# Kernel tuning notes

Measured on AMD Instinct MI355X. Metric: run time of the kernel, lower is better.

## Reference

```python
import jax, jax.numpy as jnp
import numpy as np

EPS = 1e-4
MAX_LAPLACE_VAR = 1000.0
MAX_DENSITY = 10000.0
BINS = 256

_LAP_KERNEL = jnp.array([[0., 1., 0.], [1., -4., 1.], [0., 1., 0.]], dtype=jnp.float32)[None, None]  # OIHW [1,1,3,3]


def setup_inputs() -> dict:
    key = jax.random.key(0)
    k1, k2 = jax.random.split(key)
    rgb_img = jax.random.uniform(k1, (32, 3, 512, 512), dtype=jnp.float32)
    depth_img = jax.random.normal(k2, (32, 1, 512, 512), dtype=jnp.float32)
    return {"rgb_img": rgb_img, "depth_img": depth_img}


def _rgb_confidence(rgb_img):
    B, C, H, W = rgb_img.shape
    gray = 0.299 * rgb_img[:, 0] + 0.587 * rgb_img[:, 1] + 0.114 * rgb_img[:, 2]  # [B,H,W]
    gray = gray[:, None]  # [B,1,H,W]
    lap = jax.lax.conv_general_dilated(
        gray, _LAP_KERNEL, window_strides=(1, 1), padding=[(1, 1), (1, 1)],
        dimension_numbers=("NCHW", "OIHW", "NCHW"))
    # torch.var default is unbiased (ddof=1)
    laplace_var = jnp.var(lap, axis=(1, 2, 3), ddof=1)

    # integer-valued pixels 0..255 land exactly in histc bins 0..255 (bins=256, min=0, max=255)
    vals = jnp.clip(gray * 255.0, 0.0, 255.0).astype(jnp.int32)  # [B,1,H,W]
    vals = vals.reshape(B, -1)  # [B, H*W]
    bidx = jnp.broadcast_to(jnp.arange(B)[:, None], vals.shape)
    hist = jnp.zeros((B, BINS), jnp.float32).at[bidx, vals].add(1.0)
    p = hist / jnp.sum(hist, axis=1, keepdims=True)
    entropy = -jnp.sum(p * jnp.log2(p + EPS), axis=1)

    clarity_score = laplace_var / (MAX_LAPLACE_VAR + EPS)
    uniformity_score = 1.0 / (entropy + EPS)
    return (0.5 * (clarity_score + uniformity_score))[:, None]  # [B,1]


def _depth_confidence(depth_img):
    C = depth_img.shape[1]
    depth_map = depth_img[:, 2] if C == 3 else depth_img[:, 0]  # [B,H,W]
    mask = (depth_map > 0).astype(jnp.float32)
    density = jnp.mean(mask, axis=(1, 2))

    # vectorized masked std (unbiased, ddof=1), matching torch.std over valid pixels
    n = jnp.sum(mask, axis=(1, 2))  # [B]
    mean = jnp.sum(depth_map * mask, axis=(1, 2)) / jnp.maximum(n, 1.0)
    sq = jnp.sum(mask * (depth_map - mean[:, None, None]) ** 2, axis=(1, 2))
    var = sq / jnp.maximum(n - 1.0, 1.0)
    std = jnp.sqrt(jnp.maximum(var, 0.0))
    noise_level = jnp.where(n > 0, std, 1.0)

    density_score = density / (MAX_DENSITY + EPS)
    noise_score = 1.0 / (noise_level + EPS)
    return (0.5 * (density_score + noise_score))[:, None]  # [B,1]


def reference(rgb_img, depth_img):
    rgb_conf = _rgb_confidence(rgb_img)
    depth_conf = _depth_confidence(depth_img)
    denom = rgb_conf + depth_conf + EPS
    w_r = rgb_conf / denom
    w_d = depth_conf / denom
    return (w_r, w_d)
```

## Files before the change

### kernel.cpp

```cpp
#include <hip/hip_runtime.h>

#define IMG_H 512
#define IMG_W 512
#define HW (IMG_H * IMG_W)
#define NB 32
#define STRIPS 32
#define RPW 4

#define ACCP_DOUBLES (5 * NB * STRIPS)
#define HISTP_U32 (NB * STRIPS * 256)
#define WS_BYTES (ACCP_DOUBLES * 8 + HISTP_U32 * 4)

struct Row6 { float4 a0, a1, b0, b1, c0, c1; };

__device__ inline Row6 load_row(const float* __restrict__ rp, int r, int c0) {
    Row6 x;
    if ((unsigned)r < IMG_H) {
        const size_t o = (size_t)r * IMG_W + c0;
        x.a0 = *(const float4*)(rp + o);
        x.a1 = *(const float4*)(rp + o + 4);
        x.b0 = *(const float4*)(rp + HW + o);
        x.b1 = *(const float4*)(rp + HW + o + 4);
        x.c0 = *(const float4*)(rp + 2 * HW + o);
        x.c1 = *(const float4*)(rp + 2 * HW + o + 4);
    } else {
        const float4 z = {0.f, 0.f, 0.f, 0.f};
        x.a0 = x.a1 = x.b0 = x.b1 = x.c0 = x.c1 = z;
    }
    return x;
}

__device__ inline void to_gray(const Row6& x, float g[8]) {
    g[0] = 0.299f * x.a0.x + 0.587f * x.b0.x + 0.114f * x.c0.x;
    g[1] = 0.299f * x.a0.y + 0.587f * x.b0.y + 0.114f * x.c0.y;
    g[2] = 0.299f * x.a0.z + 0.587f * x.b0.z + 0.114f * x.c0.z;
    g[3] = 0.299f * x.a0.w + 0.587f * x.b0.w + 0.114f * x.c0.w;
    g[4] = 0.299f * x.a1.x + 0.587f * x.b1.x + 0.114f * x.c1.x;
    g[5] = 0.299f * x.a1.y + 0.587f * x.b1.y + 0.114f * x.c1.y;
    g[6] = 0.299f * x.a1.z + 0.587f * x.b1.z + 0.114f * x.c1.z;
    g[7] = 0.299f * x.a1.w + 0.587f * x.b1.w + 0.114f * x.c1.w;
}

__global__ __launch_bounds__(256, 2) void fused_kernel(
    const float* __restrict__ rgb, const float* __restrict__ depth,
    double* __restrict__ accp, unsigned int* __restrict__ histp)
{
    __shared__ unsigned int lh[4][256];
    __shared__ double red[4][5];

    const int t = threadIdx.x;
    const int b = blockIdx.y;
    const int s = blockIdx.x;
    const int lane = t & 63;
    const int w = t >> 6;

    #pragma unroll
    for (int i = 0; i < 4; ++i) lh[i][t] = 0u;
    __syncthreads();

    const float* rp = rgb + (size_t)b * 3 * HW;
    const int rb = s * (4 * RPW) + w * RPW;
    const int c0 = lane * 8;

    const float4* dp = (const float4*)(depth + (size_t)b * HW + (size_t)s * (HW / STRIPS));

    Row6 r0 = load_row(rp, rb - 1, c0);
    Row6 r1 = load_row(rp, rb, c0);
    Row6 buf[3];
    float4 dv[3][2];
    buf[0] = load_row(rp, rb + 1, c0); dv[0][0] = dp[0 * 256 + t]; dv[0][1] = dp[1 * 256 + t];
    buf[1] = load_row(rp, rb + 2, c0); dv[1][0] = dp[2 * 256 + t]; dv[1][1] = dp[3 * 256 + t];
    buf[2] = load_row(rp, rb + 3, c0); dv[2][0] = dp[4 * 256 + t]; dv[2][1] = dp[5 * 256 + t];

    float gp[8], gc[8], gn[8];
    to_gray(r0, gp);
    to_gray(r1, gc);

    float s1 = 0.f, s2 = 0.f;
    float dnf = 0.f, dsf = 0.f, dqf = 0.f;

    #pragma unroll
    for (int r = 0; r < RPW; ++r) {
        const int bi = r % 3;
        to_gray(buf[bi], gn);
        const float4 d0 = dv[bi][0];
        const float4 d1 = dv[bi][1];

        if (r < RPW - 3) {
            buf[bi] = load_row(rp, rb + r + 4, c0);
            dv[bi][0] = dp[(2 * r + 6) * 256 + t];
            dv[bi][1] = dp[(2 * r + 7) * 256 + t];
        }

        float lf = __shfl_up(gc[7], 1, 64);
        if (lane == 0) lf = 0.f;
        float rt = __shfl_down(gc[0], 1, 64);
        if (lane == 63) rt = 0.f;

        #pragma unroll
        for (int j = 0; j < 8; ++j) {
            const float left  = (j == 0) ? lf : gc[j - 1];
            const float right = (j == 7) ? rt : gc[j + 1];
            const float lap = gp[j] + gn[j] + left + right - 4.f * gc[j];
            s1 += lap;
            s2 += lap * lap;
            atomicAdd(&lh[w][(int)fminf(fmaxf(gc[j] * 255.f, 0.f), 255.f)], 1u);
        }

        if (d0.x > 0.f) { dnf += 1.f; dsf += d0.x; dqf += d0.x * d0.x; }
        if (d0.y > 0.f) { dnf += 1.f; dsf += d0.y; dqf += d0.y * d0.y; }
        if (d0.z > 0.f) { dnf += 1.f; dsf += d0.z; dqf += d0.z * d0.z; }
        if (d0.w > 0.f) { dnf += 1.f; dsf += d0.w; dqf += d0.w * d0.w; }
        if (d1.x > 0.f) { dnf += 1.f; dsf += d1.x; dqf += d1.x * d1.x; }
        if (d1.y > 0.f) { dnf += 1.f; dsf += d1.y; dqf += d1.y * d1.y; }
        if (d1.z > 0.f) { dnf += 1.f; dsf += d1.z; dqf += d1.z * d1.z; }
        if (d1.w > 0.f) { dnf += 1.f; dsf += d1.w; dqf += d1.w * d1.w; }

        #pragma unroll
        for (int j = 0; j < 8; ++j) { gp[j] = gc[j]; gc[j] = gn[j]; }
    }

    double z0 = (double)s1, z1 = (double)s2, z2 = (double)dnf, z3 = (double)dsf, z4 = (double)dqf;
    for (int off = 32; off > 0; off >>= 1) {
        z0 += __shfl_down(z0, off, 64);
        z1 += __shfl_down(z1, off, 64);
        z2 += __shfl_down(z2, off, 64);
        z3 += __shfl_down(z3, off, 64);
        z4 += __shfl_down(z4, off, 64);
    }
    if (lane == 0) {
        red[w][0] = z0; red[w][1] = z1; red[w][2] = z2; red[w][3] = z3; red[w][4] = z4;
    }
    __syncthreads();

    const unsigned int hsum = lh[0][t] + lh[1][t] + lh[2][t] + lh[3][t];
    histp[((size_t)b * STRIPS + s) * 256 + t] = hsum;
    if (t < 5) {
        const double v = red[0][t] + red[1][t] + red[2][t] + red[3][t];
        accp[((size_t)t * NB + b) * STRIPS + s] = v;
    }
}

__global__ __launch_bounds__(256) void final_kernel(
    const double* __restrict__ accp,
    const unsigned int* __restrict__ histp,
    float* __restrict__ out)
{
    __shared__ float ent[4];
    __shared__ double sacc[5];

    const int t = threadIdx.x;
    const int b = blockIdx.x;
    const int lane = t & 63;
    const int w = t >> 6;

    unsigned int hv = 0u;
    #pragma unroll
    for (int s = 0; s < STRIPS; ++s)
        hv += histp[((size_t)b * STRIPS + s) * 256 + t];

    const float p = (float)hv * (1.0f / (float)HW);
    float term = p * log2f(p + 1e-4f);
    for (int off = 32; off > 0; off >>= 1) term += __shfl_down(term, off, 64);
    if (lane == 0) ent[w] = term;

    if (t < 160) {
        const int k = t >> 5, ss = t & 31;
        double v = accp[((size_t)k * NB + b) * STRIPS + ss];
        for (int off = 16; off > 0; off >>= 1) v += __shfl_down(v, off, 32);
        if (ss == 0) sacc[k] = v;
    }
    __syncthreads();

    if (t == 0) {
        const double entropy = -(double)(ent[0] + ent[1] + ent[2] + ent[3]);
        const double N = (double)HW;

        const double ls = sacc[0], lq = sacc[1];
        const double lvar = (lq - ls * ls / N) / (N - 1.0);
        const double clarity = lvar / (1000.0 + 1e-4);
        const double uniformity = 1.0 / (entropy + 1e-4);
        const double rgb_conf = 0.5 * (clarity + uniformity);

        const double n = sacc[2], sdep = sacc[3], q = sacc[4];
        const double mean = sdep / fmax(n, 1.0);
        const double sq = q - 2.0 * mean * sdep + mean * mean * n;
        const double var = sq / fmax(n - 1.0, 1.0);
        const double stdd = sqrt(fmax(var, 0.0));
        const double noise = (n > 0.0) ? stdd : 1.0;
        const double density = n / N;
        const double depth_conf = 0.5 * (density / (10000.0 + 1e-4) + 1.0 / (noise + 1e-4));

        const double denom = rgb_conf + depth_conf + 1e-4;
        out[b]      = (float)(rgb_conf / denom);
        out[NB + b] = (float)(depth_conf / denom);
    }
}

extern "C" void kernel_launch(void* const* d_in, const int* in_sizes, int n_in,
                              void* d_out, int out_size, void* d_ws, size_t ws_size,
                              hipStream_t stream) {
    const float* rgb   = (const float*)d_in[0];
    const float* depth = (const float*)d_in[1];
    float* out = (float*)d_out;

    double* accp = (double*)d_ws;
    unsigned int* histp = (unsigned int*)((char*)d_ws + ACCP_DOUBLES * 8);


    fused_kernel<<<dim3(STRIPS, NB), 256, 0, stream>>>(rgb, depth, accp, histp);
    final_kernel<<<NB, 256, 0, stream>>>(accp, histp, out);
}
```

Measured before the change: 175.4 us.

## Stage grayscale tile with halo in LDS and compute Laplacian from shared memory

Each block now loads its 16-row strip plus one halo row above and below from global memory once. It converts the pixels to grayscale and stores them in a padded LDS tile, then computes the Laplacian stencil and the histogram from LDS. Before, each wave reloaded two halo rows from global for every four rows, so about 1.5x the RGB data was read; now only 18 of every 16 rows are read. The four per-wave histograms are merged into one shared histogram, which raises atomic contention, and the depth loads are issued up front.

```diff
diff --git a/kernel.cpp b/kernel.cpp
--- a/kernel.cpp
+++ b/kernel.cpp
@@ -5,47 +5,20 @@
 #define HW (IMG_H * IMG_W)
 #define NB 32
 #define STRIPS 32
-#define RPW 4
+#define ROWS 16
+#define GROWS 18
+#define GW 520
 
 #define ACCP_DOUBLES (5 * NB * STRIPS)
 #define HISTP_U32 (NB * STRIPS * 256)
 #define WS_BYTES (ACCP_DOUBLES * 8 + HISTP_U32 * 4)
 
-struct Row6 { float4 a0, a1, b0, b1, c0, c1; };
-
-__device__ inline Row6 load_row(const float* __restrict__ rp, int r, int c0) {
-    Row6 x;
-    if ((unsigned)r < IMG_H) {
-        const size_t o = (size_t)r * IMG_W + c0;
-        x.a0 = *(const float4*)(rp + o);
-        x.a1 = *(const float4*)(rp + o + 4);
-        x.b0 = *(const float4*)(rp + HW + o);
-        x.b1 = *(const float4*)(rp + HW + o + 4);
-        x.c0 = *(const float4*)(rp + 2 * HW + o);
-        x.c1 = *(const float4*)(rp + 2 * HW + o + 4);
-    } else {
-        const float4 z = {0.f, 0.f, 0.f, 0.f};
-        x.a0 = x.a1 = x.b0 = x.b1 = x.c0 = x.c1 = z;
-    }
-    return x;
-}
-
-__device__ inline void to_gray(const Row6& x, float g[8]) {
-    g[0] = 0.299f * x.a0.x + 0.587f * x.b0.x + 0.114f * x.c0.x;
-    g[1] = 0.299f * x.a0.y + 0.587f * x.b0.y + 0.114f * x.c0.y;
-    g[2] = 0.299f * x.a0.z + 0.587f * x.b0.z + 0.114f * x.c0.z;
-    g[3] = 0.299f * x.a0.w + 0.587f * x.b0.w + 0.114f * x.c0.w;
-    g[4] = 0.299f * x.a1.x + 0.587f * x.b1.x + 0.114f * x.c1.x;
-    g[5] = 0.299f * x.a1.y + 0.587f * x.b1.y + 0.114f * x.c1.y;
-    g[6] = 0.299f * x.a1.z + 0.587f * x.b1.z + 0.114f * x.c1.z;
-    g[7] = 0.299f * x.a1.w + 0.587f * x.b1.w + 0.114f * x.c1.w;
-}
-
 __global__ __launch_bounds__(256, 2) void fused_kernel(
     const float* __restrict__ rgb, const float* __restrict__ depth,
     double* __restrict__ accp, unsigned int* __restrict__ histp)
 {
-    __shared__ unsigned int lh[4][256];
+    __shared__ float glds[GROWS * GW];
+    __shared__ unsigned int lh[256];
     __shared__ double red[4][5];
 
     const int t = threadIdx.x;
@@ -54,87 +27,99 @@
     const int lane = t & 63;
     const int w = t >> 6;
 
+    lh[t] = 0u;
+    if (t < GROWS * 8) glds[(t >> 3) * GW + 512 + (t & 7)] = 0.f;
+
+    const float* rp = rgb + (size_t)b * 3 * HW;
+    const int gr0 = s * ROWS - 1;
+
+    const float4 z4 = {0.f, 0.f, 0.f, 0.f};
     #pragma unroll
-    for (int i = 0; i < 4; ++i) lh[i][t] = 0u;
+    for (int cl = 0; cl < 3; ++cl) {
+        float4 ra[3], ga[3], ba[3];
+        int rl[3], c4[3];
+        #pragma unroll
+        for (int k = 0; k < 3; ++k) {
+            const int idx = (cl * 3 + k) * 256 + t;
+            rl[k] = idx >> 7;
+            c4[k] = idx & 127;
+            const int grow = gr0 + rl[k];
+            const bool v = (unsigned)grow < IMG_H;
+            const float* base = rp + (size_t)grow * IMG_W + 4 * c4[k];
+            ra[k] = v ? *(const float4*)(base)          : z4;
+            ga[k] = v ? *(const float4*)(base + HW)     : z4;
+            ba[k] = v ? *(const float4*)(base + 2 * HW) : z4;
+        }
+        #pragma unroll
+        for (int k = 0; k < 3; ++k) {
+            float4 gy;
+            gy.x = 0.299f * ra[k].x + 0.587f * ga[k].x + 0.114f * ba[k].x;
+            gy.y = 0.299f * ra[k].y + 0.587f * ga[k].y + 0.114f * ba[k].y;
+            gy.z = 0.299f * ra[k].z + 0.587f * ga[k].z + 0.114f * ba[k].z;
+            gy.w = 0.299f * ra[k].w + 0.587f * ga[k].w + 0.114f * ba[k].w;
+            *(float4*)(&glds[rl[k] * GW + 4 * c4[k]]) = gy;
+        }
+    }
+
+    const float4* dp = (const float4*)(depth + (size_t)b * HW + (size_t)s * (HW / STRIPS));
+    float dnf = 0.f, dsf = 0.f, dqf = 0.f;
+    {
+        float4 dv[8];
+        #pragma unroll
+        for (int k = 0; k < 8; ++k) dv[k] = dp[k * 256 + t];
+        #pragma unroll
+        for (int k = 0; k < 8; ++k) {
+            const float4 d = dv[k];
+            if (d.x > 0.f) { dnf += 1.f; dsf += d.x; dqf += d.x * d.x; }
+            if (d.y > 0.f) { dnf += 1.f; dsf += d.y; dqf += d.y * d.y; }
+            if (d.z > 0.f) { dnf += 1.f; dsf += d.z; dqf += d.z * d.z; }
+            if (d.w > 0.f) { dnf += 1.f; dsf += d.w; dqf += d.w * d.w; }
+        }
+    }
+
     __syncthreads();
 
-    const float* rp = rgb + (size_t)b * 3 * HW;
-    const int rb = s * (4 * RPW) + w * RPW;
-    const int c0 = lane * 8;
-
-    const float4* dp = (const float4*)(depth + (size_t)b * HW + (size_t)s * (HW / STRIPS));
-
-    Row6 r0 = load_row(rp, rb - 1, c0);
-    Row6 r1 = load_row(rp, rb, c0);
-    Row6 buf[3];
-    float4 dv[3][2];
-    buf[0] = load_row(rp, rb + 1, c0); dv[0][0] = dp[0 * 256 + t]; dv[0][1] = dp[1 * 256 + t];
-    buf[1] = load_row(rp, rb + 2, c0); dv[1][0] = dp[2 * 256 + t]; dv[1][1] = dp[3 * 256 + t];
-    buf[2] = load_row(rp, rb + 3, c0); dv[2][0] = dp[4 * 256 + t]; dv[2][1] = dp[5 * 256 + t];
-
-    float gp[8], gc[8], gn[8];
-    to_gray(r0, gp);
-    to_gray(r1, gc);
+    const int r_o = t >> 4;
+    const int cb = (t & 15) * 4;
+    const float* up = &glds[r_o * GW];
+    const float* ce = &glds[(r_o + 1) * GW];
+    const float* dn = &glds[(r_o + 2) * GW];
 
     float s1 = 0.f, s2 = 0.f;
-    float dnf = 0.f, dsf = 0.f, dqf = 0.f;
-
     #pragma unroll
-    for (int r = 0; r < RPW; ++r) {
-        const int bi = r % 3;
-        to_gray(buf[bi], gn);
-        const float4 d0 = dv[bi][0];
-        const float4 d1 = dv[bi][1];
-
-        if (r < RPW - 3) {
-            buf[bi] = load_row(rp, rb + r + 4, c0);
-            dv[bi][0] = dp[(2 * r + 6) * 256 + t];
-            dv[bi][1] = dp[(2 * r + 7) * 256 + t];
-        }
-
-        float lf = __shfl_up(gc[7], 1, 64);
-        if (lane == 0) lf = 0.f;
-        float rt = __shfl_down(gc[0], 1, 64);
-        if (lane == 63) rt = 0.f;
-
-        #pragma unroll
-        for (int j = 0; j < 8; ++j) {
-            const float left  = (j == 0) ? lf : gc[j - 1];
-            const float right = (j == 7) ? rt : gc[j + 1];
-            const float lap = gp[j] + gn[j] + left + right - 4.f * gc[j];
-            s1 += lap;
-            s2 += lap * lap;
-            atomicAdd(&lh[w][(int)fminf(fmaxf(gc[j] * 255.f, 0.f), 255.f)], 1u);
-        }
-
-        if (d0.x > 0.f) { dnf += 1.f; dsf += d0.x; dqf += d0.x * d0.x; }
-        if (d0.y > 0.f) { dnf += 1.f; dsf += d0.y; dqf += d0.y * d0.y; }
-        if (d0.z > 0.f) { dnf += 1.f; dsf += d0.z; dqf += d0.z * d0.z; }
-        if (d0.w > 0.f) { dnf += 1.f; dsf += d0.w; dqf += d0.w * d0.w; }
-        if (d1.x > 0.f) { dnf += 1.f; dsf += d1.x; dqf += d1.x * d1.x; }
-        if (d1.y > 0.f) { dnf += 1.f; dsf += d1.y; dqf += d1.y * d1.y; }
-        if (d1.z > 0.f) { dnf += 1.f; dsf += d1.z; dqf += d1.z * d1.z; }
-        if (d1.w > 0.f) { dnf += 1.f; dsf += d1.w; dqf += d1.w * d1.w; }
-
-        #pragma unroll
-        for (int j = 0; j < 8; ++j) { gp[j] = gc[j]; gc[j] = gn[j]; }
+    for (int k = 0; k < 8; ++k) {
+        const int c = cb + 64 * k;
+        const float4 uc = *(const float4*)(up + c);
+        const float4 cc = *(const float4*)(ce + c);
+        const float4 dc = *(const float4*)(dn + c);
+        const float lf = ce[c - 1];
+        const float rt = ce[c + 4];
+        const float l0 = uc.x + dc.x + lf   + cc.y - 4.f * cc.x;
+        const float l1 = uc.y + dc.y + cc.x + cc.z - 4.f * cc.y;
+        const float l2 = uc.z + dc.z + cc.y + cc.w - 4.f * cc.z;
+        const float l3 = uc.w + dc.w + cc.z + rt   - 4.f * cc.w;
+        s1 += l0 + l1 + l2 + l3;
+        s2 += l0 * l0 + l1 * l1 + l2 * l2 + l3 * l3;
+        atomicAdd(&lh[(int)fminf(fmaxf(cc.x * 255.f, 0.f), 255.f)], 1u);
+        atomicAdd(&lh[(int)fminf(fmaxf(cc.y * 255.f, 0.f), 255.f)], 1u);
+        atomicAdd(&lh[(int)fminf(fmaxf(cc.z * 255.f, 0.f), 255.f)], 1u);
+        atomicAdd(&lh[(int)fminf(fmaxf(cc.w * 255.f, 0.f), 255.f)], 1u);
     }
 
-    double z0 = (double)s1, z1 = (double)s2, z2 = (double)dnf, z3 = (double)dsf, z4 = (double)dqf;
+    double z0 = (double)s1, z1 = (double)s2, z2 = (double)dnf, z3 = (double)dsf, z4w = (double)dqf;
     for (int off = 32; off > 0; off >>= 1) {
         z0 += __shfl_down(z0, off, 64);
         z1 += __shfl_down(z1, off, 64);
         z2 += __shfl_down(z2, off, 64);
         z3 += __shfl_down(z3, off, 64);
-        z4 += __shfl_down(z4, off, 64);
+        z4w += __shfl_down(z4w, off, 64);
     }
     if (lane == 0) {
-        red[w][0] = z0; red[w][1] = z1; red[w][2] = z2; red[w][3] = z3; red[w][4] = z4;
+        red[w][0] = z0; red[w][1] = z1; red[w][2] = z2; red[w][3] = z3; red[w][4] = z4w;
     }
     __syncthreads();
 
-    const unsigned int hsum = lh[0][t] + lh[1][t] + lh[2][t] + lh[3][t];
-    histp[((size_t)b * STRIPS + s) * 256 + t] = hsum;
+    histp[((size_t)b * STRIPS + s) * 256 + t] = lh[t];
     if (t < 5) {
         const double v = red[0][t] + red[1][t] + red[2][t] + red[3][t];
         accp[((size_t)t * NB + b) * STRIPS + s] = v;
@@ -207,7 +192,6 @@
     double* accp = (double*)d_ws;
     unsigned int* histp = (unsigned int*)((char*)d_ws + ACCP_DOUBLES * 8);
 
-
     fused_kernel<<<dim3(STRIPS, NB), 256, 0, stream>>>(rgb, depth, accp, histp);
     final_kernel<<<NB, 256, 0, stream>>>(accp, histp, out);
 }
```

Result: slower. 182.5 us (+4.0%).
